# Kernel tuning notes

Hardware: AMD Instinct MI355X
Metric: run time of the kernel (lower is better)

## Reference

```python
import jax, jax.numpy as jnp
import numpy as np

NBINS = 256  # skimage threshold_otsu default
RGB_W = jnp.array([0.2989, 0.5870, 0.1140], dtype=jnp.float32)  # tf.image.rgb_to_grayscale weights


def threshold_otsu(img):
    """Global Otsu threshold over all pixels, matching skimage.filters.threshold_otsu."""
    vmin = img.min()
    vmax = img.max()
    edges = jnp.linspace(vmin, vmax, NBINS + 1)
    centers = (edges[:-1] + edges[1:]) * 0.5
    hist = jnp.histogram(img.ravel(), bins=edges)[0].astype(jnp.float32)
    # class probabilities / cumulative weights
    w1 = jnp.cumsum(hist)                      # weight of class <= t
    w2 = jnp.cumsum(hist[::-1])[::-1]          # weight of class > t
    hc = hist * centers
    s1 = jnp.cumsum(hc)
    s2 = jnp.cumsum(hc[::-1])[::-1]
    m1 = s1 / jnp.maximum(w1, 1.0)
    m2 = s2 / jnp.maximum(w2, 1.0)
    # inter-class variance at each split point
    var12 = w1[:-1] * w2[1:] * (m1[:-1] - m2[1:]) ** 2
    idx = jnp.argmax(var12)
    return centers[idx]


def setup_inputs() -> dict:
    key = jax.random.key(0)
    inputs = jax.random.uniform(key, (32, 128, 2048, 3), dtype=jnp.float32)
    return {"inputs": inputs}


def reference(inputs) -> jnp.ndarray:
    # rgb_to_grayscale on first 3 channels, keep channel dim -> [B,H,W,1]
    gray = jnp.einsum('bhwc,c->bhw', inputs[..., :3].astype(jnp.float32), RGB_W)[..., None]
    thresh = threshold_otsu(gray)
    binarized = (gray > thresh).astype(jnp.float32)   # [B,H,W,1]
    # channels == 3 -> tile grayscale binarization back to 3 channels
    binarized = jnp.tile(binarized, (1, 1, 1, 3))
    return binarized
```

## Files before the change

kernel.cpp:

```cpp
#include <hip/hip_runtime.h>

static constexpr int HIST_OFF    = 2;
static constexpr int EDGES_OFF   = 258;
static constexpr int VMIN_OFF    = 515;
static constexpr int DELTA_OFF   = 516;
static constexpr int INVD_OFF    = 517;
static constexpr int THRESH_OFF  = 518;
static constexpr int SCRATCH_OFF = 1024;
static constexpr size_t GRAY_BYTE_OFF = 32768;

typedef float nfloat4 __attribute__((ext_vector_type(4)));

__device__ __forceinline__ unsigned fkey(float x) {
    unsigned u = __float_as_uint(x);
    return (u & 0x80000000u) ? ~u : (u | 0x80000000u);
}
__device__ __forceinline__ float keyf(unsigned k) {
    return (k & 0x80000000u) ? __uint_as_float(k & 0x7FFFFFFFu)
                             : __uint_as_float(~k);
}
__device__ __forceinline__ float gray1(float r, float g, float b) {
    float t0 = __fmul_rn(r, 0.2989f);
    float t1 = __fmul_rn(g, 0.5870f);
    float t2 = __fmul_rn(b, 0.1140f);
    return __fadd_rn(__fadd_rn(t0, t1), t2);
}

__global__ void init_kernel(unsigned* __restrict__ wsu) {
    int i = threadIdx.x;
    if (i < 256) wsu[HIST_OFF + i] = 0u;
    if (i == 0) { wsu[0] = 0xFFFFFFFFu; wsu[1] = 0u; }
}

__global__ void __launch_bounds__(256)
gray_minmax_lds(const float* __restrict__ in, float* __restrict__ gray,
                unsigned* __restrict__ wsu, int npix4) {
    __shared__ float4 sb[4][2][192];
    __shared__ unsigned smn[4], smx[4];
    const float4* __restrict__ in4 = (const float4*)in;
    float4* __restrict__ gray4 = (float4*)gray;
    const int lane = threadIdx.x & 63;
    const int w = threadIdx.x >> 6;
    const int gw = blockIdx.x * 4 + w;
    const size_t base = (size_t)gw * 768;
    unsigned mn = 0xFFFFFFFFu, mx = 0u;

    float4 a0 = in4[base + lane];
    float4 a1 = in4[base + 64 + lane];
    float4 a2 = in4[base + 128 + lane];
    __builtin_amdgcn_sched_barrier(0);
    sb[w][0][lane]       = a0;
    sb[w][0][64 + lane]  = a1;
    sb[w][0][128 + lane] = a2;
    a0 = in4[base + 192 + lane];
    a1 = in4[base + 256 + lane];
    a2 = in4[base + 320 + lane];
    __builtin_amdgcn_sched_barrier(0);

#pragma unroll
    for (int t = 0; t < 4; ++t) {
        const int cb = t & 1;
        float4 c0 = sb[w][cb][3 * lane + 0];
        float4 c1 = sb[w][cb][3 * lane + 1];
        float4 c2 = sb[w][cb][3 * lane + 2];
        float g0 = gray1(c0.x, c0.y, c0.z);
        float g1 = gray1(c0.w, c1.x, c1.y);
        float g2 = gray1(c1.z, c1.w, c2.x);
        float g3 = gray1(c2.y, c2.z, c2.w);
        gray4[(size_t)gw * 256 + t * 64 + lane] = make_float4(g0, g1, g2, g3);
        unsigned k0 = fkey(g0), k1 = fkey(g1), k2 = fkey(g2), k3 = fkey(g3);
        mn = min(mn, min(min(k0, k1), min(k2, k3)));
        mx = max(mx, max(max(k0, k1), max(k2, k3)));
        if (t < 3) {
            sb[w][cb ^ 1][lane]       = a0;
            sb[w][cb ^ 1][64 + lane]  = a1;
            sb[w][cb ^ 1][128 + lane] = a2;
            if (t < 2) {
                a0 = in4[base + (size_t)(t + 2) * 192 + lane];
                a1 = in4[base + (size_t)(t + 2) * 192 + 64 + lane];
                a2 = in4[base + (size_t)(t + 2) * 192 + 128 + lane];
            }
            __builtin_amdgcn_sched_barrier(0);
        }
    }
    for (int off = 32; off > 0; off >>= 1) {
        mn = min(mn, (unsigned)__shfl_xor((int)mn, off, 64));
        mx = max(mx, (unsigned)__shfl_xor((int)mx, off, 64));
    }
    if (lane == 0) { smn[w] = mn; smx[w] = mx; }
    __syncthreads();
    if (threadIdx.x == 0) {
        mn = min(min(smn[0], smn[1]), min(smn[2], smn[3]));
        mx = max(max(smx[0], smx[1]), max(smx[2], smx[3]));
        wsu[SCRATCH_OFF + 2 * blockIdx.x]     = mn;
        wsu[SCRATCH_OFF + 2 * blockIdx.x + 1] = mx;
    }
}

__global__ void __launch_bounds__(256)
gray_minmax_generic(const float* __restrict__ in, float* __restrict__ gray,
                    unsigned* __restrict__ wsu, int npix4) {
    __shared__ unsigned smn[4], smx[4];
    const float4* in4 = (const float4*)in;
    const int stride = gridDim.x * blockDim.x;
    unsigned mn = 0xFFFFFFFFu, mx = 0u;
    for (int t = blockIdx.x * blockDim.x + threadIdx.x; t < npix4; t += stride) {
        const float4* p = in4 + (size_t)t * 3;
        float4 c0 = p[0], c1 = p[1], c2 = p[2];
        float g0 = gray1(c0.x, c0.y, c0.z);
        float g1 = gray1(c0.w, c1.x, c1.y);
        float g2 = gray1(c1.z, c1.w, c2.x);
        float g3 = gray1(c2.y, c2.z, c2.w);
        if (gray) ((float4*)gray)[t] = make_float4(g0, g1, g2, g3);
        unsigned k0 = fkey(g0), k1 = fkey(g1), k2 = fkey(g2), k3 = fkey(g3);
        mn = min(mn, min(min(k0, k1), min(k2, k3)));
        mx = max(mx, max(max(k0, k1), max(k2, k3)));
    }
    for (int off = 32; off > 0; off >>= 1) {
        mn = min(mn, (unsigned)__shfl_xor((int)mn, off, 64));
        mx = max(mx, (unsigned)__shfl_xor((int)mx, off, 64));
    }
    int wave = threadIdx.x >> 6;
    if ((threadIdx.x & 63) == 0) { smn[wave] = mn; smx[wave] = mx; }
    __syncthreads();
    if (threadIdx.x == 0) {
        mn = min(min(smn[0], smn[1]), min(smn[2], smn[3]));
        mx = max(max(smx[0], smx[1]), max(smx[2], smx[3]));
        atomicMin(&wsu[0], mn);
        atomicMax(&wsu[1], mx);
    }
}

__global__ void edges_kernel(unsigned* __restrict__ wsu,
                             float* __restrict__ wsf, int nblk) {
    __shared__ unsigned rmn[4], rmx[4];
    const int i = threadIdx.x;
    unsigned mn = 0xFFFFFFFFu, mx = 0u;
    if (nblk > 0) {
        for (int b = i; b < nblk; b += 256) {
            mn = min(mn, wsu[SCRATCH_OFF + 2 * b]);
            mx = max(mx, wsu[SCRATCH_OFF + 2 * b + 1]);
        }
        for (int off = 32; off > 0; off >>= 1) {
            mn = min(mn, (unsigned)__shfl_xor((int)mn, off, 64));
            mx = max(mx, (unsigned)__shfl_xor((int)mx, off, 64));
        }
        const int w = i >> 6;
        if ((i & 63) == 0) { rmn[w] = mn; rmx[w] = mx; }
        __syncthreads();
        mn = min(min(rmn[0], rmn[1]), min(rmn[2], rmn[3]));
        mx = max(max(rmx[0], rmx[1]), max(rmx[2], rmx[3]));
    } else {
        mn = wsu[0];
        mx = wsu[1];
    }
    const float vmin = keyf(mn);
    const float vmax = keyf(mx);
    const float delta = __fdiv_rn(__fsub_rn(vmax, vmin), 256.0f);
    wsf[EDGES_OFF + i] = __fadd_rn(vmin, __fmul_rn((float)i, delta));
    if (i == 0) {
        wsf[EDGES_OFF + 256] = vmax;
        wsf[VMIN_OFF]  = vmin;
        wsf[DELTA_OFF] = delta;
        wsf[INVD_OFF]  = (delta > 0.0f) ? __fdiv_rn(1.0f, delta) : 0.0f;
    }
}

__device__ __forceinline__ void bin4(float x0, float x1, float x2, float x3,
                                     const float* eds, float vmin, float invd,
                                     unsigned* lh) {
    float xs[4] = {x0, x1, x2, x3};
#pragma unroll
    for (int j = 0; j < 4; ++j) {
        float x = xs[j];
        int b = (int)(__fmul_rn(__fsub_rn(x, vmin), invd));
        b = b < 0 ? 0 : (b > 255 ? 255 : b);
        while (b < 255 && x >= eds[b + 1]) ++b;
        while (b > 0 && x < eds[b]) --b;
        atomicAdd(&lh[b], 1u);
    }
}

__global__ void __launch_bounds__(256)
hist_kernel(const float* __restrict__ gray, const float* __restrict__ in,
            const float* __restrict__ wsf, unsigned* __restrict__ wsu,
            int npix4) {
    __shared__ float eds[257];
    __shared__ unsigned lh[256];
    for (int i = threadIdx.x; i < 257; i += blockDim.x)
        eds[i] = wsf[EDGES_OFF + i];
    if (threadIdx.x < 256) lh[threadIdx.x] = 0u;
    __syncthreads();
    const float vmin = eds[0];
    const float invd = wsf[INVD_OFF];
    const int stride = gridDim.x * blockDim.x;
    const int base = blockIdx.x * blockDim.x + threadIdx.x;
    if (gray && base + 7 * stride < npix4) {
        float4 g[8];
#pragma unroll
        for (int j = 0; j < 8; ++j) g[j] = ((const float4*)gray)[base + j * stride];
#pragma unroll
        for (int j = 0; j < 8; ++j)
            bin4(g[j].x, g[j].y, g[j].z, g[j].w, eds, vmin, invd, lh);
    } else {
        for (int t = base; t < npix4; t += stride) {
            float4 g4;
            if (gray) g4 = ((const float4*)gray)[t];
            else {
                const float4* p = (const float4*)in + (size_t)t * 3;
                float4 c0 = p[0], c1 = p[1], c2 = p[2];
                g4 = make_float4(gray1(c0.x, c0.y, c0.z), gray1(c0.w, c1.x, c1.y),
                                 gray1(c1.z, c1.w, c2.x), gray1(c2.y, c2.z, c2.w));
            }
            bin4(g4.x, g4.y, g4.z, g4.w, eds, vmin, invd, lh);
        }
    }
    __syncthreads();
    if (threadIdx.x < 256 && lh[threadIdx.x] != 0u)
        atomicAdd(&wsu[HIST_OFF + threadIdx.x], lh[threadIdx.x]);
}

__global__ void otsu_kernel(const unsigned* __restrict__ wsu,
                            float* __restrict__ wsf) {
    __shared__ float histf[256];
    __shared__ float centers[256];
    __shared__ float w2a[256];
    __shared__ float s2a[256];
    int i = threadIdx.x;
    float e0 = wsf[EDGES_OFF + i];
    float e1 = wsf[EDGES_OFF + i + 1];
    centers[i] = __fmul_rn(__fadd_rn(e0, e1), 0.5f);
    histf[i] = (float)wsu[HIST_OFF + i];
    __syncthreads();
    if (i == 0) {
        float w = 0.0f, s = 0.0f;
        for (int t = 255; t >= 0; --t) {
            w = __fadd_rn(w, histf[t]);
            s = __fadd_rn(s, __fmul_rn(histf[t], centers[t]));
            w2a[t] = w;
            s2a[t] = s;
        }
        float w1 = 0.0f, s1 = 0.0f, best = -1.0f;
        int bidx = 0;
        for (int t = 0; t < 255; ++t) {
            w1 = __fadd_rn(w1, histf[t]);
            s1 = __fadd_rn(s1, __fmul_rn(histf[t], centers[t]));
            float m1 = __fdiv_rn(s1, fmaxf(w1, 1.0f));
            float m2 = __fdiv_rn(s2a[t + 1], fmaxf(w2a[t + 1], 1.0f));
            float d  = __fsub_rn(m1, m2);
            float v  = __fmul_rn(__fmul_rn(w1, w2a[t + 1]), __fmul_rn(d, d));
            if (v > best) { best = v; bidx = t; }
        }
        wsf[THRESH_OFF] = centers[bidx];
    }
}

__global__ void __launch_bounds__(256)
binarize_fast(const float* __restrict__ gray, const float* __restrict__ wsf,
              float* __restrict__ out, int npix4) {
    const float thr = wsf[THRESH_OFF];
    const nfloat4* gray4 = (const nfloat4*)gray;
    nfloat4* out4 = (nfloat4*)out;
    const int lane = threadIdx.x & 63;
    const int gw = (blockIdx.x * blockDim.x + threadIdx.x) >> 6;
    const int ma = lane / 3,         qa = lane % 3;
    const int mb = (64 + lane) / 3,  qb = (64 + lane) % 3;
    const int mc = (128 + lane) / 3, qc = (128 + lane) % 3;

    nfloat4 g[4];
    bool full[4];
#pragma unroll
    for (int r = 0; r < 4; ++r) {
        int gbase = gw * 256 + r * 64;
        full[r] = (gbase + 64 <= npix4);
        if (full[r]) g[r] = gray4[gbase + lane];
    }
#pragma unroll
    for (int r = 0; r < 4; ++r) {
        const int gbase = gw * 256 + r * 64;
        if (full[r]) {
            unsigned u = (g[r].x > thr ? 1u : 0u) |
                         (g[r].y > thr ? 0x100u : 0u) |
                         (g[r].z > thr ? 0x10000u : 0u) |
                         (g[r].w > thr ? 0x1000000u : 0u);
            const int rb = 3 * gbase;
#pragma unroll
            for (int k = 0; k < 3; ++k) {
                int m = (k == 0) ? ma : (k == 1) ? mb : mc;
                int q = (k == 0) ? qa : (k == 1) ? qb : qc;
                unsigned w = (unsigned)__builtin_amdgcn_ds_bpermute(4 * m,
                                                                    (int)u);
                float h0 = (w & 0xffu)       ? 1.0f : 0.0f;
                float h1 = (w & 0xff00u)     ? 1.0f : 0.0f;
                float h2 = (w & 0xff0000u)   ? 1.0f : 0.0f;
                float h3 = (w & 0xff000000u) ? 1.0f : 0.0f;
                nfloat4 o;
                o.x = (q == 0) ? h0 : (q == 1) ? h1 : h2;
                o.y = (q == 0) ? h0 : (q == 1) ? h1 : h3;
                o.z = (q == 0) ? h0 : (q == 1) ? h2 : h3;
                o.w = (q == 0) ? h1 : (q == 1) ? h2 : h3;
                __builtin_nontemporal_store(o, &out4[rb + 64 * k + lane]);
            }
        } else {
            int t = gbase + lane;
            if (t < npix4) {
                nfloat4 gg = gray4[t];
                float b0 = (gg.x > thr) ? 1.0f : 0.0f;
                float b1 = (gg.y > thr) ? 1.0f : 0.0f;
                float b2 = (gg.z > thr) ? 1.0f : 0.0f;
                float b3 = (gg.w > thr) ? 1.0f : 0.0f;
                nfloat4* o = out4 + (size_t)t * 3;
                __builtin_nontemporal_store((nfloat4){b0, b0, b0, b1}, &o[0]);
                __builtin_nontemporal_store((nfloat4){b1, b1, b2, b2}, &o[1]);
                __builtin_nontemporal_store((nfloat4){b2, b3, b3, b3}, &o[2]);
            }
        }
    }
}

__global__ void __launch_bounds__(256)
binarize_generic(const float* __restrict__ gray, const float* __restrict__ in,
                 const float* __restrict__ wsf, float* __restrict__ out,
                 int npix4) {
    const float thr = wsf[THRESH_OFF];
    const int stride = gridDim.x * blockDim.x;
    nfloat4* out4 = (nfloat4*)out;
    for (int t = blockIdx.x * blockDim.x + threadIdx.x; t < npix4; t += stride) {
        float4 g4;
        if (gray) g4 = ((const float4*)gray)[t];
        else {
            const float4* p = (const float4*)in + (size_t)t * 3;
            float4 c0 = p[0], c1 = p[1], c2 = p[2];
            g4 = make_float4(gray1(c0.x, c0.y, c0.z), gray1(c0.w, c1.x, c1.y),
                             gray1(c1.z, c1.w, c2.x), gray1(c2.y, c2.z, c2.w));
        }
        float b0 = (g4.x > thr) ? 1.0f : 0.0f;
        float b1 = (g4.y > thr) ? 1.0f : 0.0f;
        float b2 = (g4.z > thr) ? 1.0f : 0.0f;
        float b3 = (g4.w > thr) ? 1.0f : 0.0f;
        nfloat4* o = out4 + (size_t)t * 3;
        o[0] = (nfloat4){b0, b0, b0, b1};
        o[1] = (nfloat4){b1, b1, b2, b2};
        o[2] = (nfloat4){b2, b3, b3, b3};
    }
}

extern "C" void kernel_launch(void* const* d_in, const int* in_sizes, int n_in,
                              void* d_out, int out_size, void* d_ws,
                              size_t ws_size, hipStream_t stream) {
    const float* in = (const float*)d_in[0];
    float* out = (float*)d_out;
    int npix  = out_size / 3;
    int npix4 = npix / 4;
    unsigned* wsu = (unsigned*)d_ws;
    float* wsf = (float*)d_ws;
    size_t need = GRAY_BYTE_OFF + (size_t)npix * sizeof(float);
    float* gray = (ws_size >= need)
                      ? (float*)((char*)d_ws + GRAY_BYTE_OFF)
                      : nullptr;

    hipLaunchKernelGGL(init_kernel, dim3(1), dim3(256), 0, stream, wsu);
    int nblk = 0;
    if (gray && npix4 % 1024 == 0) {
        nblk = npix4 / 1024;
        hipLaunchKernelGGL(gray_minmax_lds, dim3(nblk), dim3(256), 0,
                           stream, in, gray, wsu, npix4);
    } else {
        hipLaunchKernelGGL(gray_minmax_generic, dim3(2048), dim3(256), 0,
                           stream, in, gray, wsu, npix4);
    }
    hipLaunchKernelGGL(edges_kernel, dim3(1), dim3(256), 0, stream, wsu, wsf,
                       nblk);
    hipLaunchKernelGGL(hist_kernel, dim3(1024), dim3(256), 0, stream,
                       gray, in, wsf, wsu, npix4);
    hipLaunchKernelGGL(otsu_kernel, dim3(1), dim3(256), 0, stream, wsu, wsf);
    if (gray) {
        hipLaunchKernelGGL(binarize_fast, dim3((npix4 + 1023) / 1024),
                           dim3(256), 0, stream, gray, wsf, out, npix4);
    } else {
        hipLaunchKernelGGL(binarize_generic, dim3(2048), dim3(256), 0, stream,
                           gray, in, wsf, out, npix4);
    }
}
```

Baseline: 259.3 us.

## Fuse whole Otsu pipeline into one cooperative kernel keeping gray in registers

```diff
diff --git a/kernel.cpp b/kernel.cpp
--- a/kernel.cpp
+++ b/kernel.cpp
@@ -1,4 +1,7 @@
 #include <hip/hip_runtime.h>
+#include <hip/hip_cooperative_groups.h>
+
+namespace cg = cooperative_groups;
 
 static constexpr int HIST_OFF    = 2;
 static constexpr int EDGES_OFF   = 258;
@@ -25,6 +28,189 @@
     float t2 = __fmul_rn(b, 0.1140f);
     return __fadd_rn(__fadd_rn(t0, t1), t2);
 }
+
+__device__ __forceinline__ void bin4(float x0, float x1, float x2, float x3,
+                                     const float* eds, float vmin, float invd,
+                                     unsigned* lh) {
+    float xs[4] = {x0, x1, x2, x3};
+#pragma unroll
+    for (int j = 0; j < 4; ++j) {
+        float x = xs[j];
+        int b = (int)(__fmul_rn(__fsub_rn(x, vmin), invd));
+        b = b < 0 ? 0 : (b > 255 ? 255 : b);
+        while (b < 255 && x >= eds[b + 1]) ++b;
+        while (b > 0 && x < eds[b]) --b;
+        atomicAdd(&lh[b], 1u);
+    }
+}
+
+__global__ void __launch_bounds__(256, 4)
+fused_otsu(const float* __restrict__ in, float* __restrict__ out,
+           unsigned* __restrict__ wsu, float* __restrict__ wsf, int nblk) {
+    __shared__ float eds[257];
+    __shared__ unsigned lh[256];
+    __shared__ float histf[256], centers[256];
+    __shared__ float w1a[256], s1a[256], w2a[256], s2a[256];
+    __shared__ unsigned rmn[4], rmx[4];
+    __shared__ float rbv[4];
+    __shared__ int rbi[4];
+    __shared__ float sthresh;
+
+    const int t = threadIdx.x;
+    const int lane = t & 63;
+    const int w = t >> 6;
+    const int b = blockIdx.x;
+    const float4* __restrict__ in4 = (const float4*)in;
+    nfloat4* __restrict__ out4 = (nfloat4*)out;
+    const int base0 = b * 2048;
+
+    nfloat4 g[8];
+    unsigned mn = 0xFFFFFFFFu, mx = 0u;
+#pragma unroll
+    for (int r = 0; r < 8; ++r) {
+        const int idx = base0 + r * 256 + t;
+        const float4* p = in4 + 3 * (size_t)idx;
+        float4 c0 = p[0], c1 = p[1], c2 = p[2];
+        float g0 = gray1(c0.x, c0.y, c0.z);
+        float g1 = gray1(c0.w, c1.x, c1.y);
+        float g2 = gray1(c1.z, c1.w, c2.x);
+        float g3 = gray1(c2.y, c2.z, c2.w);
+        g[r].x = g0; g[r].y = g1; g[r].z = g2; g[r].w = g3;
+        unsigned k0 = fkey(g0), k1 = fkey(g1), k2 = fkey(g2), k3 = fkey(g3);
+        mn = min(mn, min(min(k0, k1), min(k2, k3)));
+        mx = max(mx, max(max(k0, k1), max(k2, k3)));
+    }
+    if (b == 0)
+        __hip_atomic_store(&wsu[HIST_OFF + t], 0u, __ATOMIC_RELAXED,
+                           __HIP_MEMORY_SCOPE_AGENT);
+    for (int off = 32; off > 0; off >>= 1) {
+        mn = min(mn, (unsigned)__shfl_xor((int)mn, off, 64));
+        mx = max(mx, (unsigned)__shfl_xor((int)mx, off, 64));
+    }
+    if (lane == 0) { rmn[w] = mn; rmx[w] = mx; }
+    __syncthreads();
+    if (t == 0) {
+        mn = min(min(rmn[0], rmn[1]), min(rmn[2], rmn[3]));
+        mx = max(max(rmx[0], rmx[1]), max(rmx[2], rmx[3]));
+        __hip_atomic_store(&wsu[SCRATCH_OFF + 2 * b], mn, __ATOMIC_RELAXED,
+                           __HIP_MEMORY_SCOPE_AGENT);
+        __hip_atomic_store(&wsu[SCRATCH_OFF + 2 * b + 1], mx, __ATOMIC_RELAXED,
+                           __HIP_MEMORY_SCOPE_AGENT);
+    }
+    cg::this_grid().sync();
+
+    mn = 0xFFFFFFFFu; mx = 0u;
+    for (int i = t; i < nblk; i += 256) {
+        mn = min(mn, __hip_atomic_load(&wsu[SCRATCH_OFF + 2 * i],
+                                       __ATOMIC_RELAXED,
+                                       __HIP_MEMORY_SCOPE_AGENT));
+        mx = max(mx, __hip_atomic_load(&wsu[SCRATCH_OFF + 2 * i + 1],
+                                       __ATOMIC_RELAXED,
+                                       __HIP_MEMORY_SCOPE_AGENT));
+    }
+    for (int off = 32; off > 0; off >>= 1) {
+        mn = min(mn, (unsigned)__shfl_xor((int)mn, off, 64));
+        mx = max(mx, (unsigned)__shfl_xor((int)mx, off, 64));
+    }
+    if (lane == 0) { rmn[w] = mn; rmx[w] = mx; }
+    __syncthreads();
+    mn = min(min(rmn[0], rmn[1]), min(rmn[2], rmn[3]));
+    mx = max(max(rmx[0], rmx[1]), max(rmx[2], rmx[3]));
+    const float vmin = keyf(mn);
+    const float vmax = keyf(mx);
+    const float delta = __fdiv_rn(__fsub_rn(vmax, vmin), 256.0f);
+    const float invd = (delta > 0.0f) ? __fdiv_rn(1.0f, delta) : 0.0f;
+    eds[t] = __fadd_rn(vmin, __fmul_rn((float)t, delta));
+    if (t == 0) eds[256] = vmax;
+    lh[t] = 0u;
+    __syncthreads();
+
+#pragma unroll
+    for (int r = 0; r < 8; ++r)
+        bin4(g[r].x, g[r].y, g[r].z, g[r].w, eds, vmin, invd, lh);
+    __syncthreads();
+    if (lh[t] != 0u) atomicAdd(&wsu[HIST_OFF + t], lh[t]);
+    cg::this_grid().sync();
+
+    histf[t] = (float)__hip_atomic_load(&wsu[HIST_OFF + t], __ATOMIC_RELAXED,
+                                        __HIP_MEMORY_SCOPE_AGENT);
+    centers[t] = __fmul_rn(__fadd_rn(eds[t], eds[t + 1]), 0.5f);
+    __syncthreads();
+    if (t == 0) {
+        float ww = 0.0f, ss = 0.0f;
+        for (int k = 255; k >= 0; --k) {
+            ww = __fadd_rn(ww, histf[k]);
+            ss = __fadd_rn(ss, __fmul_rn(histf[k], centers[k]));
+            w2a[k] = ww;
+            s2a[k] = ss;
+        }
+        ww = 0.0f; ss = 0.0f;
+        for (int k = 0; k < 255; ++k) {
+            ww = __fadd_rn(ww, histf[k]);
+            ss = __fadd_rn(ss, __fmul_rn(histf[k], centers[k]));
+            w1a[k] = ww;
+            s1a[k] = ss;
+        }
+    }
+    __syncthreads();
+    float v = -1.0f;
+    int ti = 256;
+    if (t < 255) {
+        float m1 = __fdiv_rn(s1a[t], fmaxf(w1a[t], 1.0f));
+        float m2 = __fdiv_rn(s2a[t + 1], fmaxf(w2a[t + 1], 1.0f));
+        float d  = __fsub_rn(m1, m2);
+        v  = __fmul_rn(__fmul_rn(w1a[t], w2a[t + 1]), __fmul_rn(d, d));
+        ti = t;
+    }
+    for (int off = 32; off > 0; off >>= 1) {
+        float ov = __shfl_xor(v, off, 64);
+        int oi = __shfl_xor(ti, off, 64);
+        if (ov > v || (ov == v && oi < ti)) { v = ov; ti = oi; }
+    }
+    if (lane == 0) { rbv[w] = v; rbi[w] = ti; }
+    __syncthreads();
+    if (t == 0) {
+        float bv = rbv[0]; int bi = rbi[0];
+        for (int k = 1; k < 4; ++k)
+            if (rbv[k] > bv || (rbv[k] == bv && rbi[k] < bi)) {
+                bv = rbv[k]; bi = rbi[k];
+            }
+        sthresh = centers[bi];
+        if (b == 0) wsf[THRESH_OFF] = centers[bi];
+    }
+    __syncthreads();
+    const float thr = sthresh;
+
+    const int ma = lane / 3,         qa = lane % 3;
+    const int mb = (64 + lane) / 3,  qb = (64 + lane) % 3;
+    const int mc = (128 + lane) / 3, qc = (128 + lane) % 3;
+#pragma unroll
+    for (int r = 0; r < 8; ++r) {
+        unsigned u = (g[r].x > thr ? 1u : 0u) |
+                     (g[r].y > thr ? 0x100u : 0u) |
+                     (g[r].z > thr ? 0x10000u : 0u) |
+                     (g[r].w > thr ? 0x1000000u : 0u);
+        const int wavebase = base0 + r * 256 + w * 64;
+        const size_t rb = 3 * (size_t)wavebase;
+#pragma unroll
+        for (int k = 0; k < 3; ++k) {
+            int m = (k == 0) ? ma : (k == 1) ? mb : mc;
+            int q = (k == 0) ? qa : (k == 1) ? qb : qc;
+            unsigned x = (unsigned)__builtin_amdgcn_ds_bpermute(4 * m, (int)u);
+            float h0 = (x & 0xffu)       ? 1.0f : 0.0f;
+            float h1 = (x & 0xff00u)     ? 1.0f : 0.0f;
+            float h2 = (x & 0xff0000u)   ? 1.0f : 0.0f;
+            float h3 = (x & 0xff000000u) ? 1.0f : 0.0f;
+            nfloat4 o;
+            o.x = (q == 0) ? h0 : (q == 1) ? h1 : h2;
+            o.y = (q == 0) ? h0 : (q == 1) ? h1 : h3;
+            o.z = (q == 0) ? h0 : (q == 1) ? h2 : h3;
+            o.w = (q == 0) ? h1 : (q == 1) ? h2 : h3;
+            __builtin_nontemporal_store(o, &out4[rb + 64 * k + lane]);
+        }
+    }
+}
+
 
 __global__ void init_kernel(unsigned* __restrict__ wsu) {
     int i = threadIdx.x;
@@ -166,21 +352,6 @@
     }
 }
 
-__device__ __forceinline__ void bin4(float x0, float x1, float x2, float x3,
-                                     const float* eds, float vmin, float invd,
-                                     unsigned* lh) {
-    float xs[4] = {x0, x1, x2, x3};
-#pragma unroll
-    for (int j = 0; j < 4; ++j) {
-        float x = xs[j];
-        int b = (int)(__fmul_rn(__fsub_rn(x, vmin), invd));
-        b = b < 0 ? 0 : (b > 255 ? 255 : b);
-        while (b < 255 && x >= eds[b + 1]) ++b;
-        while (b > 0 && x < eds[b]) --b;
-        atomicAdd(&lh[b], 1u);
-    }
-}
-
 __global__ void __launch_bounds__(256)
 hist_kernel(const float* __restrict__ gray, const float* __restrict__ in,
             const float* __restrict__ wsf, unsigned* __restrict__ wsu,
@@ -288,12 +459,12 @@
             for (int k = 0; k < 3; ++k) {
                 int m = (k == 0) ? ma : (k == 1) ? mb : mc;
                 int q = (k == 0) ? qa : (k == 1) ? qb : qc;
-                unsigned w = (unsigned)__builtin_amdgcn_ds_bpermute(4 * m,
+                unsigned x = (unsigned)__builtin_amdgcn_ds_bpermute(4 * m,
                                                                     (int)u);
-                float h0 = (w & 0xffu)       ? 1.0f : 0.0f;
-                float h1 = (w & 0xff00u)     ? 1.0f : 0.0f;
-                float h2 = (w & 0xff0000u)   ? 1.0f : 0.0f;
-                float h3 = (w & 0xff000000u) ? 1.0f : 0.0f;
+                float h0 = (x & 0xffu)       ? 1.0f : 0.0f;
+                float h1 = (x & 0xff00u)     ? 1.0f : 0.0f;
+                float h2 = (x & 0xff0000u)   ? 1.0f : 0.0f;
+                float h3 = (x & 0xff000000u) ? 1.0f : 0.0f;
                 nfloat4 o;
                 o.x = (q == 0) ? h0 : (q == 1) ? h1 : h2;
                 o.y = (q == 0) ? h0 : (q == 1) ? h1 : h3;
@@ -345,6 +516,33 @@
     }
 }
 
+static void launch_fallback(const float* in, float* out, unsigned* wsu,
+                            float* wsf, float* gray, int npix4,
+                            hipStream_t stream) {
+    hipLaunchKernelGGL(init_kernel, dim3(1), dim3(256), 0, stream, wsu);
+    int nblk = 0;
+    if (gray && npix4 % 1024 == 0) {
+        nblk = npix4 / 1024;
+        hipLaunchKernelGGL(gray_minmax_lds, dim3(nblk), dim3(256), 0,
+                           stream, in, gray, wsu, npix4);
+    } else {
+        hipLaunchKernelGGL(gray_minmax_generic, dim3(2048), dim3(256), 0,
+                           stream, in, gray, wsu, npix4);
+    }
+    hipLaunchKernelGGL(edges_kernel, dim3(1), dim3(256), 0, stream, wsu, wsf,
+                       nblk);
+    hipLaunchKernelGGL(hist_kernel, dim3(1024), dim3(256), 0, stream,
+                       gray, in, wsf, wsu, npix4);
+    hipLaunchKernelGGL(otsu_kernel, dim3(1), dim3(256), 0, stream, wsu, wsf);
+    if (gray) {
+        hipLaunchKernelGGL(binarize_fast, dim3((npix4 + 1023) / 1024),
+                           dim3(256), 0, stream, gray, wsf, out, npix4);
+    } else {
+        hipLaunchKernelGGL(binarize_generic, dim3(2048), dim3(256), 0, stream,
+                           gray, in, wsf, out, npix4);
+    }
+}
+
 extern "C" void kernel_launch(void* const* d_in, const int* in_sizes, int n_in,
                               void* d_out, int out_size, void* d_ws,
                               size_t ws_size, hipStream_t stream) {
@@ -359,26 +557,28 @@
                       ? (float*)((char*)d_ws + GRAY_BYTE_OFF)
                       : nullptr;
 
-    hipLaunchKernelGGL(init_kernel, dim3(1), dim3(256), 0, stream, wsu);
-    int nblk = 0;
-    if (gray && npix4 % 1024 == 0) {
-        nblk = npix4 / 1024;
-        hipLaunchKernelGGL(gray_minmax_lds, dim3(nblk), dim3(256), 0,
-                           stream, in, gray, wsu, npix4);
-    } else {
-        hipLaunchKernelGGL(gray_minmax_generic, dim3(2048), dim3(256), 0,
-                           stream, in, gray, wsu, npix4);
-    }
-    hipLaunchKernelGGL(edges_kernel, dim3(1), dim3(256), 0, stream, wsu, wsf,
-                       nblk);
-    hipLaunchKernelGGL(hist_kernel, dim3(1024), dim3(256), 0, stream,
-                       gray, in, wsf, wsu, npix4);
-    hipLaunchKernelGGL(otsu_kernel, dim3(1), dim3(256), 0, stream, wsu, wsf);
-    if (gray) {
-        hipLaunchKernelGGL(binarize_fast, dim3((npix4 + 1023) / 1024),
-                           dim3(256), 0, stream, gray, wsf, out, npix4);
-    } else {
-        hipLaunchKernelGGL(binarize_generic, dim3(2048), dim3(256), 0, stream,
-                           gray, in, wsf, out, npix4);
-    }
-}
+    static int capacity = -2;
+    if (capacity == -2) {
+        capacity = -1;
+        int dev = 0, nb = 0;
+        hipDeviceProp_t prop;
+        if (hipGetDevice(&dev) == hipSuccess &&
+            hipGetDeviceProperties(&prop, dev) == hipSuccess &&
+            hipOccupancyMaxActiveBlocksPerMultiprocessor(
+                &nb, (const void*)fused_otsu, 256, 0) == hipSuccess)
+            capacity = nb * prop.multiProcessorCount;
+    }
+
+    const int NB = npix4 / 2048;
+    const bool fused_ok = (npix4 % 2048 == 0) && NB >= 1 && capacity >= NB &&
+                          ws_size >= (size_t)4096 + 8u * (size_t)NB;
+    if (fused_ok) {
+        int nb_arg = NB;
+        void* args[] = {(void*)&in, (void*)&out, (void*)&wsu, (void*)&wsf,
+                        (void*)&nb_arg};
+        hipError_t e = hipLaunchCooperativeKernel(
+            (const void*)fused_otsu, dim3(NB), dim3(256), args, 0, stream);
+        if (e == hipSuccess) return;
+    }
+    launch_fallback(in, out, wsu, wsf, gray, npix4, stream);
+}
```

Result: no change. 259.0 us (-0.1%).

## Fuse tiny edges/otsu kernels into histogram and binarize kernels, cutting launches

Applied to the files above, without the earlier changes.

```diff
diff --git a/kernel.cpp b/kernel.cpp
--- a/kernel.cpp
+++ b/kernel.cpp
@@ -26,11 +26,41 @@
     return __fadd_rn(__fadd_rn(t0, t1), t2);
 }
 
-__global__ void init_kernel(unsigned* __restrict__ wsu) {
-    int i = threadIdx.x;
-    if (i < 256) wsu[HIST_OFF + i] = 0u;
-    if (i == 0) { wsu[0] = 0xFFFFFFFFu; wsu[1] = 0u; }
-}
+__device__ __forceinline__ void bin4(float x0, float x1, float x2, float x3,
+                                     const float* eds, float vmin, float invd,
+                                     unsigned* lh) {
+    float xs[4] = {x0, x1, x2, x3};
+#pragma unroll
+    for (int j = 0; j < 4; ++j) {
+        float x = xs[j];
+        int b = (int)(__fmul_rn(__fsub_rn(x, vmin), invd));
+        b = b < 0 ? 0 : (b > 255 ? 255 : b);
+        while (b < 255 && x >= eds[b + 1]) ++b;
+        while (b > 0 && x < eds[b]) --b;
+        atomicAdd(&lh[b], 1u);
+    }
+}
+
+__device__ __forceinline__ void reduce_pairs(const unsigned* __restrict__ wsu,
+                                             int npairs, int t,
+                                             unsigned& mn, unsigned& mx,
+                                             unsigned* rmn, unsigned* rmx) {
+    mn = 0xFFFFFFFFu; mx = 0u;
+    for (int i = t; i < npairs; i += 256) {
+        mn = min(mn, wsu[SCRATCH_OFF + 2 * i]);
+        mx = max(mx, wsu[SCRATCH_OFF + 2 * i + 1]);
+    }
+    for (int off = 32; off > 0; off >>= 1) {
+        mn = min(mn, (unsigned)__shfl_xor((int)mn, off, 64));
+        mx = max(mx, (unsigned)__shfl_xor((int)mx, off, 64));
+    }
+    const int w = t >> 6;
+    if ((t & 63) == 0) { rmn[w] = mn; rmx[w] = mx; }
+    __syncthreads();
+    mn = min(min(rmn[0], rmn[1]), min(rmn[2], rmn[3]));
+    mx = max(max(rmx[0], rmx[1]), max(rmx[2], rmx[3]));
+}
+
 
 __global__ void __launch_bounds__(256)
 gray_minmax_lds(const float* __restrict__ in, float* __restrict__ gray,
@@ -44,6 +74,8 @@
     const int gw = blockIdx.x * 4 + w;
     const size_t base = (size_t)gw * 768;
     unsigned mn = 0xFFFFFFFFu, mx = 0u;
+
+    if (blockIdx.x == 0) wsu[HIST_OFF + threadIdx.x] = 0u;
 
     float4 a0 = in4[base + lane];
     float4 a1 = in4[base + 64 + lane];
@@ -98,6 +130,146 @@
 }
 
 __global__ void __launch_bounds__(256)
+hist_fused(const float* __restrict__ gray, unsigned* __restrict__ wsu,
+           int npairs, int npix4) {
+    __shared__ float eds[257];
+    __shared__ unsigned lh[256];
+    __shared__ unsigned rmn[4], rmx[4];
+    const int t = threadIdx.x;
+    unsigned mn, mx;
+    reduce_pairs(wsu, npairs, t, mn, mx, rmn, rmx);
+    const float vmin = keyf(mn);
+    const float vmax = keyf(mx);
+    const float delta = __fdiv_rn(__fsub_rn(vmax, vmin), 256.0f);
+    const float invd = (delta > 0.0f) ? __fdiv_rn(1.0f, delta) : 0.0f;
+    eds[t] = __fadd_rn(vmin, __fmul_rn((float)t, delta));
+    if (t == 0) eds[256] = vmax;
+    lh[t] = 0u;
+    __syncthreads();
+
+    const int stride = gridDim.x * 256;
+    const int base = blockIdx.x * 256 + t;
+    float4 g[8];
+#pragma unroll
+    for (int j = 0; j < 8; ++j) g[j] = ((const float4*)gray)[base + j * stride];
+#pragma unroll
+    for (int j = 0; j < 8; ++j)
+        bin4(g[j].x, g[j].y, g[j].z, g[j].w, eds, vmin, invd, lh);
+    __syncthreads();
+    if (lh[t] != 0u) atomicAdd(&wsu[HIST_OFF + t], lh[t]);
+}
+
+__global__ void __launch_bounds__(256)
+binarize_fused(const float* __restrict__ gray, const unsigned* __restrict__ wsu,
+               float* __restrict__ out, int npairs, int npix4) {
+    __shared__ float eds[257];
+    __shared__ float histf[256], centers[256];
+    __shared__ float w1a[256], s1a[256], w2a[256], s2a[256];
+    __shared__ unsigned rmn[4], rmx[4];
+    __shared__ float rbv[4];
+    __shared__ int rbi[4];
+    __shared__ float sthresh;
+    const int t = threadIdx.x;
+    const int lane = t & 63;
+    const int w = t >> 6;
+
+    unsigned mn, mx;
+    reduce_pairs(wsu, npairs, t, mn, mx, rmn, rmx);
+    const float vmin = keyf(mn);
+    const float vmax = keyf(mx);
+    const float delta = __fdiv_rn(__fsub_rn(vmax, vmin), 256.0f);
+    eds[t] = __fadd_rn(vmin, __fmul_rn((float)t, delta));
+    if (t == 0) eds[256] = vmax;
+    histf[t] = (float)wsu[HIST_OFF + t];
+    __syncthreads();
+    centers[t] = __fmul_rn(__fadd_rn(eds[t], eds[t + 1]), 0.5f);
+    __syncthreads();
+    if (t == 0) {
+        float ww = 0.0f, ss = 0.0f;
+        for (int k = 255; k >= 0; --k) {
+            ww = __fadd_rn(ww, histf[k]);
+            ss = __fadd_rn(ss, __fmul_rn(histf[k], centers[k]));
+            w2a[k] = ww;
+            s2a[k] = ss;
+        }
+        ww = 0.0f; ss = 0.0f;
+        for (int k = 0; k < 255; ++k) {
+            ww = __fadd_rn(ww, histf[k]);
+            ss = __fadd_rn(ss, __fmul_rn(histf[k], centers[k]));
+            w1a[k] = ww;
+            s1a[k] = ss;
+        }
+    }
+    __syncthreads();
+    float v = -1.0f;
+    int ti = 256;
+    if (t < 255) {
+        float m1 = __fdiv_rn(s1a[t], fmaxf(w1a[t], 1.0f));
+        float m2 = __fdiv_rn(s2a[t + 1], fmaxf(w2a[t + 1], 1.0f));
+        float d  = __fsub_rn(m1, m2);
+        v  = __fmul_rn(__fmul_rn(w1a[t], w2a[t + 1]), __fmul_rn(d, d));
+        ti = t;
+    }
+    for (int off = 32; off > 0; off >>= 1) {
+        float ov = __shfl_xor(v, off, 64);
+        int oi = __shfl_xor(ti, off, 64);
+        if (ov > v || (ov == v && oi < ti)) { v = ov; ti = oi; }
+    }
+    if (lane == 0) { rbv[w] = v; rbi[w] = ti; }
+    __syncthreads();
+    if (t == 0) {
+        float bv = rbv[0]; int bi = rbi[0];
+        for (int k = 1; k < 4; ++k)
+            if (rbv[k] > bv || (rbv[k] == bv && rbi[k] < bi)) {
+                bv = rbv[k]; bi = rbi[k];
+            }
+        sthresh = centers[bi];
+    }
+    __syncthreads();
+    const float thr = sthresh;
+
+    const nfloat4* gray4 = (const nfloat4*)gray;
+    nfloat4* out4 = (nfloat4*)out;
+    const int gw = blockIdx.x * 4 + w;
+    const int ma = lane / 3,         qa = lane % 3;
+    const int mb = (64 + lane) / 3,  qb = (64 + lane) % 3;
+    const int mc = (128 + lane) / 3, qc = (128 + lane) % 3;
+#pragma unroll
+    for (int r = 0; r < 8; ++r) {
+        const int gbase = gw * 512 + r * 64;
+        nfloat4 gg = gray4[gbase + lane];
+        unsigned u = (gg.x > thr ? 1u : 0u) |
+                     (gg.y > thr ? 0x100u : 0u) |
+                     (gg.z > thr ? 0x10000u : 0u) |
+                     (gg.w > thr ? 0x1000000u : 0u);
+        const size_t rb = 3 * (size_t)gbase;
+#pragma unroll
+        for (int k = 0; k < 3; ++k) {
+            int m = (k == 0) ? ma : (k == 1) ? mb : mc;
+            int q = (k == 0) ? qa : (k == 1) ? qb : qc;
+            unsigned x = (unsigned)__builtin_amdgcn_ds_bpermute(4 * m, (int)u);
+            float h0 = (x & 0xffu)       ? 1.0f : 0.0f;
+            float h1 = (x & 0xff00u)     ? 1.0f : 0.0f;
+            float h2 = (x & 0xff0000u)   ? 1.0f : 0.0f;
+            float h3 = (x & 0xff000000u) ? 1.0f : 0.0f;
+            nfloat4 o;
+            o.x = (q == 0) ? h0 : (q == 1) ? h1 : h2;
+            o.y = (q == 0) ? h0 : (q == 1) ? h1 : h3;
+            o.z = (q == 0) ? h0 : (q == 1) ? h2 : h3;
+            o.w = (q == 0) ? h1 : (q == 1) ? h2 : h3;
+            __builtin_nontemporal_store(o, &out4[rb + 64 * k + lane]);
+        }
+    }
+}
+
+
+__global__ void init_kernel(unsigned* __restrict__ wsu) {
+    int i = threadIdx.x;
+    if (i < 256) wsu[HIST_OFF + i] = 0u;
+    if (i == 0) { wsu[0] = 0xFFFFFFFFu; wsu[1] = 0u; }
+}
+
+__global__ void __launch_bounds__(256)
 gray_minmax_generic(const float* __restrict__ in, float* __restrict__ gray,
                     unsigned* __restrict__ wsu, int npix4) {
     __shared__ unsigned smn[4], smx[4];
@@ -166,21 +338,6 @@
     }
 }
 
-__device__ __forceinline__ void bin4(float x0, float x1, float x2, float x3,
-                                     const float* eds, float vmin, float invd,
-                                     unsigned* lh) {
-    float xs[4] = {x0, x1, x2, x3};
-#pragma unroll
-    for (int j = 0; j < 4; ++j) {
-        float x = xs[j];
-        int b = (int)(__fmul_rn(__fsub_rn(x, vmin), invd));
-        b = b < 0 ? 0 : (b > 255 ? 255 : b);
-        while (b < 255 && x >= eds[b + 1]) ++b;
-        while (b > 0 && x < eds[b]) --b;
-        atomicAdd(&lh[b], 1u);
-    }
-}
-
 __global__ void __launch_bounds__(256)
 hist_kernel(const float* __restrict__ gray, const float* __restrict__ in,
             const float* __restrict__ wsf, unsigned* __restrict__ wsu,
@@ -195,25 +352,16 @@
     const float invd = wsf[INVD_OFF];
     const int stride = gridDim.x * blockDim.x;
     const int base = blockIdx.x * blockDim.x + threadIdx.x;
-    if (gray && base + 7 * stride < npix4) {
-        float4 g[8];
-#pragma unroll
-        for (int j = 0; j < 8; ++j) g[j] = ((const float4*)gray)[base + j * stride];
-#pragma unroll
-        for (int j = 0; j < 8; ++j)
-            bin4(g[j].x, g[j].y, g[j].z, g[j].w, eds, vmin, invd, lh);
-    } else {
-        for (int t = base; t < npix4; t += stride) {
-            float4 g4;
-            if (gray) g4 = ((const float4*)gray)[t];
-            else {
-                const float4* p = (const float4*)in + (size_t)t * 3;
-                float4 c0 = p[0], c1 = p[1], c2 = p[2];
-                g4 = make_float4(gray1(c0.x, c0.y, c0.z), gray1(c0.w, c1.x, c1.y),
-                                 gray1(c1.z, c1.w, c2.x), gray1(c2.y, c2.z, c2.w));
-            }
-            bin4(g4.x, g4.y, g4.z, g4.w, eds, vmin, invd, lh);
-        }
+    for (int t = base; t < npix4; t += stride) {
+        float4 g4;
+        if (gray) g4 = ((const float4*)gray)[t];
+        else {
+            const float4* p = (const float4*)in + (size_t)t * 3;
+            float4 c0 = p[0], c1 = p[1], c2 = p[2];
+            g4 = make_float4(gray1(c0.x, c0.y, c0.z), gray1(c0.w, c1.x, c1.y),
+                             gray1(c1.z, c1.w, c2.x), gray1(c2.y, c2.z, c2.w));
+        }
+        bin4(g4.x, g4.y, g4.z, g4.w, eds, vmin, invd, lh);
     }
     __syncthreads();
     if (threadIdx.x < 256 && lh[threadIdx.x] != 0u)
@@ -252,69 +400,6 @@
             if (v > best) { best = v; bidx = t; }
         }
         wsf[THRESH_OFF] = centers[bidx];
-    }
-}
-
-__global__ void __launch_bounds__(256)
-binarize_fast(const float* __restrict__ gray, const float* __restrict__ wsf,
-              float* __restrict__ out, int npix4) {
-    const float thr = wsf[THRESH_OFF];
-    const nfloat4* gray4 = (const nfloat4*)gray;
-    nfloat4* out4 = (nfloat4*)out;
-    const int lane = threadIdx.x & 63;
-    const int gw = (blockIdx.x * blockDim.x + threadIdx.x) >> 6;
-    const int ma = lane / 3,         qa = lane % 3;
-    const int mb = (64 + lane) / 3,  qb = (64 + lane) % 3;
-    const int mc = (128 + lane) / 3, qc = (128 + lane) % 3;
-
-    nfloat4 g[4];
-    bool full[4];
-#pragma unroll
-    for (int r = 0; r < 4; ++r) {
-        int gbase = gw * 256 + r * 64;
-        full[r] = (gbase + 64 <= npix4);
-        if (full[r]) g[r] = gray4[gbase + lane];
-    }
-#pragma unroll
-    for (int r = 0; r < 4; ++r) {
-        const int gbase = gw * 256 + r * 64;
-        if (full[r]) {
-            unsigned u = (g[r].x > thr ? 1u : 0u) |
-                         (g[r].y > thr ? 0x100u : 0u) |
-                         (g[r].z > thr ? 0x10000u : 0u) |
-                         (g[r].w > thr ? 0x1000000u : 0u);
-            const int rb = 3 * gbase;
-#pragma unroll
-            for (int k = 0; k < 3; ++k) {
-                int m = (k == 0) ? ma : (k == 1) ? mb : mc;
-                int q = (k == 0) ? qa : (k == 1) ? qb : qc;
-                unsigned w = (unsigned)__builtin_amdgcn_ds_bpermute(4 * m,
-                                                                    (int)u);
-                float h0 = (w & 0xffu)       ? 1.0f : 0.0f;
-                float h1 = (w & 0xff00u)     ? 1.0f : 0.0f;
-                float h2 = (w & 0xff0000u)   ? 1.0f : 0.0f;
-                float h3 = (w & 0xff000000u) ? 1.0f : 0.0f;
-                nfloat4 o;
-                o.x = (q == 0) ? h0 : (q == 1) ? h1 : h2;
-                o.y = (q == 0) ? h0 : (q == 1) ? h1 : h3;
-                o.z = (q == 0) ? h0 : (q == 1) ? h2 : h3;
-                o.w = (q == 0) ? h1 : (q == 1) ? h2 : h3;
-                __builtin_nontemporal_store(o, &out4[rb + 64 * k + lane]);
-            }
-        } else {
-            int t = gbase + lane;
-            if (t < npix4) {
-                nfloat4 gg = gray4[t];
-                float b0 = (gg.x > thr) ? 1.0f : 0.0f;
-                float b1 = (gg.y > thr) ? 1.0f : 0.0f;
-                float b2 = (gg.z > thr) ? 1.0f : 0.0f;
-                float b3 = (gg.w > thr) ? 1.0f : 0.0f;
-                nfloat4* o = out4 + (size_t)t * 3;
-                __builtin_nontemporal_store((nfloat4){b0, b0, b0, b1}, &o[0]);
-                __builtin_nontemporal_store((nfloat4){b1, b1, b2, b2}, &o[1]);
-                __builtin_nontemporal_store((nfloat4){b2, b3, b3, b3}, &o[2]);
-            }
-        }
     }
 }
 
@@ -345,6 +430,21 @@
     }
 }
 
+static void launch_fallback(const float* in, float* out, unsigned* wsu,
+                            float* wsf, float* gray, int npix4,
+                            hipStream_t stream) {
+    hipLaunchKernelGGL(init_kernel, dim3(1), dim3(256), 0, stream, wsu);
+    hipLaunchKernelGGL(gray_minmax_generic, dim3(2048), dim3(256), 0,
+                       stream, in, gray, wsu, npix4);
+    hipLaunchKernelGGL(edges_kernel, dim3(1), dim3(256), 0, stream, wsu, wsf,
+                       0);
+    hipLaunchKernelGGL(hist_kernel, dim3(1024), dim3(256), 0, stream,
+                       gray, in, wsf, wsu, npix4);
+    hipLaunchKernelGGL(otsu_kernel, dim3(1), dim3(256), 0, stream, wsu, wsf);
+    hipLaunchKernelGGL(binarize_generic, dim3(2048), dim3(256), 0, stream,
+                       gray, in, wsf, out, npix4);
+}
+
 extern "C" void kernel_launch(void* const* d_in, const int* in_sizes, int n_in,
                               void* d_out, int out_size, void* d_ws,
                               size_t ws_size, hipStream_t stream) {
@@ -359,26 +459,17 @@
                       ? (float*)((char*)d_ws + GRAY_BYTE_OFF)
                       : nullptr;
 
-    hipLaunchKernelGGL(init_kernel, dim3(1), dim3(256), 0, stream, wsu);
-    int nblk = 0;
-    if (gray && npix4 % 1024 == 0) {
-        nblk = npix4 / 1024;
-        hipLaunchKernelGGL(gray_minmax_lds, dim3(nblk), dim3(256), 0,
+    const bool fast = gray && (npix4 % 2048 == 0);
+    if (fast) {
+        const int npairs = npix4 / 1024;
+        const int nb2 = npix4 / 2048;
+        hipLaunchKernelGGL(gray_minmax_lds, dim3(npairs), dim3(256), 0,
                            stream, in, gray, wsu, npix4);
+        hipLaunchKernelGGL(hist_fused, dim3(nb2), dim3(256), 0, stream,
+                           gray, wsu, npairs, npix4);
+        hipLaunchKernelGGL(binarize_fused, dim3(nb2), dim3(256), 0, stream,
+                           gray, wsu, out, npairs, npix4);
     } else {
-        hipLaunchKernelGGL(gray_minmax_generic, dim3(2048), dim3(256), 0,
-                           stream, in, gray, wsu, npix4);
-    }
-    hipLaunchKernelGGL(edges_kernel, dim3(1), dim3(256), 0, stream, wsu, wsf,
-                       nblk);
-    hipLaunchKernelGGL(hist_kernel, dim3(1024), dim3(256), 0, stream,
-                       gray, in, wsf, wsu, npix4);
-    hipLaunchKernelGGL(otsu_kernel, dim3(1), dim3(256), 0, stream, wsu, wsf);
-    if (gray) {
-        hipLaunchKernelGGL(binarize_fast, dim3((npix4 + 1023) / 1024),
-                           dim3(256), 0, stream, gray, wsf, out, npix4);
-    } else {
-        hipLaunchKernelGGL(binarize_generic, dim3(2048), dim3(256), 0, stream,
-                           gray, in, wsf, out, npix4);
-    }
-}
+        launch_fallback(in, out, wsu, wsf, gray, npix4, stream);
+    }
+}
```

New measurement: 237.8 us. -8.3%, faster.
